# Kernel optimization log

Hardware: AMD Instinct MI355X
Metric: run time of the kernel (lower is better)

The kernel has to match this reference:

```python
import jax, jax.numpy as jnp
import numpy as np

N_NODES = 50000
N_EDGES = 800000
N_GRAPHS = 64
F0 = 64          # num_features
HID = 512        # hidden_size
N_OUT = 1


def setup_inputs() -> dict:
    key = jax.random.key(0)
    ks = jax.random.split(key, 16)

    def p(k, shape, scale):
        return jax.random.normal(k, shape, jnp.float32) * scale

    inp = {}
    inp["feature"] = jax.random.normal(ks[0], (N_NODES, F0), jnp.float32)
    inp["edge_index"] = jax.random.randint(ks[1], (2, N_EDGES), 0, N_NODES)
    inp["protein_batch"] = jnp.sort(jax.random.randint(ks[2], (N_NODES,), 0, N_GRAPHS))

    dims = [(F0, F0), (F0, 2 * F0), (2 * F0, 4 * F0)]
    for i, (din, dout) in enumerate(dims):
        s = 1.0 / np.sqrt(din)
        inp[f"W{i+1}"] = p(ks[3 + 3 * i], (din, dout), s)      # GATConv lin weight
        inp[f"att{i+1}"] = p(ks[4 + 3 * i], (2, dout), 0.1)    # [att_src; att_dst]
        inp[f"b{i+1}"] = jnp.zeros((dout,), jnp.float32)       # GATConv bias
    inp["fc1_w"] = p(ks[12], (4 * F0, HID), 1.0 / np.sqrt(4 * F0))
    inp["fc1_b"] = jnp.zeros((HID,), jnp.float32)
    inp["fc2_w"] = p(ks[13], (HID, N_OUT), 1.0 / np.sqrt(HID))
    inp["fc2_b"] = jnp.zeros((N_OUT,), jnp.float32)
    return inp


def _gat_conv(x, src, dst, W, att, b):
    """PyG GATConv, heads=1, concat=True, negative_slope=0.2 (self-loops already in src/dst)."""
    h = x @ W                                             # [N, Dout]
    # per-edge attention logit: a_src . h_j + a_dst . h_i
    alpha = jax.nn.leaky_relu(h @ att[0], 0.2 * 0 + 0.0)  # placeholder, replaced below
    logit = jax.nn.leaky_relu((h @ att[0])[src] + (h @ att[1])[dst], negative_slope=0.2)  # [E]
    # segment softmax over edges grouped by destination node
    m = jax.ops.segment_max(logit, dst, num_segments=N_NODES)      # [N]
    e = jnp.exp(logit - m[dst])                                    # [E]
    s = jax.ops.segment_sum(e, dst, num_segments=N_NODES)          # [N]
    coef = e / s[dst]                                              # [E]
    out = jax.ops.segment_sum(coef[:, None] * h[src], dst, num_segments=N_NODES)  # [N, Dout]
    return out + b


def reference(feature, edge_index, protein_batch,
              W1, att1, b1, W2, att2, b2, W3, att3, b3,
              fc1_w, fc1_b, fc2_w, fc2_b):
    loop = jnp.arange(N_NODES)
    src = jnp.concatenate([edge_index[0], loop])   # add_self_loops=True
    dst = jnp.concatenate([edge_index[1], loop])

    x = jax.nn.relu(_gat_conv(feature, src, dst, W1, att1, b1))
    x = jax.nn.relu(_gat_conv(x, src, dst, W2, att2, b2))
    x = jax.nn.relu(_gat_conv(x, src, dst, W3, att3, b3))

    # global mean pool per graph
    sums = jax.ops.segment_sum(x, protein_batch, num_segments=N_GRAPHS)          # [G, 4F]
    cnts = jax.ops.segment_sum(jnp.ones((N_NODES,), x.dtype), protein_batch,
                               num_segments=N_GRAPHS)                            # [G]
    gc = sums / jnp.maximum(cnts, 1.0)[:, None]

    gc = jax.nn.relu(gc @ fc1_w + fc1_b)   # dropout is identity at inference
    return gc @ fc2_w + fc2_b
```

## Files before the change

kernel.cpp:

```cpp
#include <hip/hip_runtime.h>
#include <hip/hip_bf16.h>

#define N_NODES 50000
#define N_EDGES 800000
#define E_TOT   850000
#define N_GRAPHS 64
#define HID 512

typedef unsigned short u16;
typedef __attribute__((ext_vector_type(8))) short short8;
typedef __attribute__((ext_vector_type(4))) float floatx4;
typedef union { uint4 u; short8 s; } frag_u;

__device__ inline unsigned f2b(float x) {
    unsigned u = __float_as_uint(x);
    return (u + 0x7fffu + ((u >> 16) & 1u)) >> 16;
}
__device__ inline float b2f_lo(unsigned u) { return __uint_as_float(u << 16); }
__device__ inline float b2f_hi(unsigned u) { return __uint_as_float(u & 0xffff0000u); }

__global__ __launch_bounds__(256) void count_kernel(const int* __restrict__ dst_e,
                                                    int* __restrict__ cnt,
                                                    int* __restrict__ order) {
    int e = blockIdx.x * 256 + threadIdx.x;
    if (e >= E_TOT) return;
    int d = (e < N_EDGES) ? dst_e[e] : (e - N_EDGES);
    order[e] = atomicAdd(&cnt[d], 1);
}

__global__ __launch_bounds__(256) void scan_local(const int* __restrict__ cnt,
                                                  int* __restrict__ out,
                                                  int* __restrict__ blocksum, int n) {
    __shared__ int buf[256];
    int tid = threadIdx.x;
    int i = blockIdx.x * 256 + tid;
    int v = (i < n) ? cnt[i] : 0;
    buf[tid] = v;
    __syncthreads();
    for (int off = 1; off < 256; off <<= 1) {
        int t = (tid >= off) ? buf[tid - off] : 0;
        __syncthreads();
        buf[tid] += t;
        __syncthreads();
    }
    if (i < n) out[i] = buf[tid] - v;
    if (tid == 255) blocksum[blockIdx.x] = buf[255];
}

__global__ __launch_bounds__(256) void scan_block(const int* __restrict__ blocksum,
                                                  int* __restrict__ blockoff, int nb,
                                                  int* __restrict__ total_ptr) {
    __shared__ int buf[256];
    int tid = threadIdx.x;
    int v = (tid < nb) ? blocksum[tid] : 0;
    buf[tid] = v;
    __syncthreads();
    for (int off = 1; off < 256; off <<= 1) {
        int t = (tid >= off) ? buf[tid - off] : 0;
        __syncthreads();
        buf[tid] += t;
        __syncthreads();
    }
    blockoff[tid] = buf[tid] - v;
    if (tid == 255) *total_ptr = buf[255];
}

__global__ __launch_bounds__(256) void scan_add(int* __restrict__ row_ptr,
                                                const int* __restrict__ blockoff, int n) {
    int i = blockIdx.x * 256 + threadIdx.x;
    if (i < n) row_ptr[i] += blockoff[blockIdx.x];
}

__global__ __launch_bounds__(256) void fill_kernel(const int* __restrict__ edge_index,
                                                   const int* __restrict__ row_ptr,
                                                   const int* __restrict__ order,
                                                   int* __restrict__ col_idx) {
    int e = blockIdx.x * 256 + threadIdx.x;
    if (e >= E_TOT) return;
    int s, d;
    if (e < N_EDGES) { s = edge_index[e]; d = edge_index[N_EDGES + e]; }
    else             { s = e - N_EDGES;   d = s; }
    col_idx[row_ptr[d] + order[e]] = s;
}

struct PrepDesc {
    const float* W[3];
    const float* att[3];
    float* wsd[3];
    u16* Wt[3];
};

__global__ __launch_bounds__(256) void prep_kernel(PrepDesc d) {
    const int DIN[3]  = {64, 64, 128};
    const int DOUT[3] = {64, 128, 256};
    int b = blockIdx.x;
    if (b < 128) {
        int wg = (b * 256 + (int)threadIdx.x) >> 6;
        int lane = threadIdx.x & 63;
        int l = (wg < 128) ? 0 : (wg < 256) ? 1 : 2;
        int base = (l == 0) ? 0 : (l == 1) ? 128 : 256;
        int k = wg - base;
        int Din = DIN[l], Dout = DOUT[l];
        int half = (k >= Din) ? 1 : 0;
        int row = half ? (k - Din) : k;
        float s = 0.f;
        for (int j = lane; j < Dout; j += 64)
            s += d.W[l][(size_t)row * Dout + j] * d.att[l][half * Dout + j];
#pragma unroll
        for (int off = 32; off > 0; off >>= 1) s += __shfl_xor(s, off);
        if (lane == 0) d.wsd[l][k] = s;
    } else {
        int t = (b - 128) * 256 + (int)threadIdx.x;
        int l; int off;
        if (t < 4096)       { l = 0; off = t; }
        else if (t < 12288) { l = 1; off = t - 4096; }
        else if (t < 45056) { l = 2; off = t - 12288; }
        else return;
        int Din = DIN[l], Dout = DOUT[l];
        int row = off / Dout, j = off & (Dout - 1);
        d.Wt[l][(size_t)j * Din + row] = (u16)f2b(d.W[l][off]);
    }
}

__global__ __launch_bounds__(256) void cvt_lsld_kernel(const float* __restrict__ feature,
                                                       const float* __restrict__ wsd,
                                                       u16* __restrict__ Fb,
                                                       float* __restrict__ lsld) {
    int wid = (blockIdx.x * 256 + threadIdx.x) >> 6;
    int lane = threadIdx.x & 63;
    if (wid >= N_NODES) return;
    float h = feature[(size_t)wid * 64 + lane];
    float a0 = h * wsd[lane];
    float a1 = h * wsd[64 + lane];
#pragma unroll
    for (int off = 32; off > 0; off >>= 1) {
        a0 += __shfl_xor(a0, off);
        a1 += __shfl_xor(a1, off);
    }
    if (lane == 0) { lsld[wid] = a0; lsld[N_NODES + wid] = a1; }
    Fb[(size_t)wid * 64 + lane] = (u16)f2b(h);
}

template <int NN, int KK>
__global__ __launch_bounds__(256) void sgemm_mfma_kernel(const u16* __restrict__ A,
                                                         const u16* __restrict__ Bt,
                                                         u16* __restrict__ C,
                                                         const float* __restrict__ bias,
                                                         const float* __restrict__ wsd_next,
                                                         float* __restrict__ lsld_next,
                                                         const int* __restrict__ batch,
                                                         float* __restrict__ gsum_pool,
                                                         int M) {
    constexpr int NT = 4;
    constexpr int KSTEPS = KK / 32;
    constexpr int CS = 72;
    __shared__ u16 cst[4][32 * CS];
    const int lane = threadIdx.x & 63;
    const int w = threadIdx.x >> 6;
    const int c = lane & 15;
    const int q = lane >> 4;
    const int bn = blockIdx.y * 64;
    const int r0 = blockIdx.x * 128 + w * 32;
    int ar0 = r0 + c;      if (ar0 > M - 1) ar0 = M - 1;
    int ar1 = r0 + 16 + c; if (ar1 > M - 1) ar1 = M - 1;
    const u16* __restrict__ Ap0 = A + (size_t)ar0 * KK + q * 8;
    const u16* __restrict__ Ap1 = A + (size_t)ar1 * KK + q * 8;
    floatx4 acc[2][NT];
#pragma unroll
    for (int i = 0; i < 2; ++i)
#pragma unroll
        for (int b = 0; b < NT; ++b) acc[i][b] = (floatx4){0.f, 0.f, 0.f, 0.f};
#pragma unroll
    for (int ks = 0; ks < KSTEPS; ++ks) {
        const int k0 = ks * 32;
        frag_u a0, a1, bf[NT];
        a0.u = *(const uint4*)(Ap0 + k0);
        a1.u = *(const uint4*)(Ap1 + k0);
#pragma unroll
        for (int b = 0; b < NT; ++b)
            bf[b].u = *(const uint4*)(Bt + (size_t)(bn + b * 16 + c) * KK + q * 8 + k0);
#pragma unroll
        for (int b = 0; b < NT; ++b) {
            acc[0][b] = __builtin_amdgcn_mfma_f32_16x16x32_bf16(a0.s, bf[b].s, acc[0][b], 0, 0, 0);
            acc[1][b] = __builtin_amdgcn_mfma_f32_16x16x32_bf16(a1.s, bf[b].s, acc[1][b], 0, 0, 0);
        }
    }

    if (gsum_pool) {
        float bsv[NT];
#pragma unroll
        for (int b = 0; b < NT; ++b) bsv[b] = bias[bn + b * 16 + c];
        const bool full = (r0 + 31 < M);
        const int rl = full ? (r0 + 31) : (M - 1);
        if (full && batch[r0] == batch[rl]) {
            const int gr = batch[r0];
#pragma unroll
            for (int b = 0; b < NT; ++b) {
                float s = 0.f;
#pragma unroll
                for (int i = 0; i < 2; ++i)
#pragma unroll
                    for (int g = 0; g < 4; ++g) s += fmaxf(acc[i][b][g] + bsv[b], 0.f);
                s += __shfl_xor(s, 16);
                s += __shfl_xor(s, 32);
                if (q == 0) atomicAdd(&gsum_pool[gr * 256 + bn + b * 16 + c], s);
            }
        } else {
#pragma unroll
            for (int i = 0; i < 2; ++i) {
                int curg = -1;
                float sb[NT] = {0.f, 0.f, 0.f, 0.f};
#pragma unroll
                for (int g = 0; g < 4; ++g) {
                    int r = r0 + i * 16 + q * 4 + g;
                    if (r < M) {
                        int gr = batch[r];
                        if (gr != curg) {
                            if (curg >= 0) {
#pragma unroll
                                for (int b = 0; b < NT; ++b) {
                                    atomicAdd(&gsum_pool[curg * 256 + bn + b * 16 + c], sb[b]);
                                    sb[b] = 0.f;
                                }
                            }
                            curg = gr;
                        }
#pragma unroll
                        for (int b = 0; b < NT; ++b) sb[b] += fmaxf(acc[i][b][g] + bsv[b], 0.f);
                    }
                }
                if (curg >= 0) {
#pragma unroll
                    for (int b = 0; b < NT; ++b)
                        atomicAdd(&gsum_pool[curg * 256 + bn + b * 16 + c], sb[b]);
                }
            }
        }
        return;
    }

    const bool has_next = (wsd_next != nullptr);
    u16* __restrict__ cb = cst[w];
    float ps[2][4] = {}, pd[2][4] = {};
#pragma unroll
    for (int b = 0; b < NT; ++b) {
        const int col = bn + b * 16 + c;
        const float bsv = bias[col];
        const float wsv = has_next ? wsd_next[col] : 0.f;
        const float wdv = has_next ? wsd_next[NN + col] : 0.f;
#pragma unroll
        for (int i = 0; i < 2; ++i) {
#pragma unroll
            for (int g = 0; g < 4; ++g) {
                float v = fmaxf(acc[i][b][g] + bsv, 0.f);
                cb[(i * 16 + q * 4 + g) * CS + b * 16 + c] = (u16)f2b(v);
                ps[i][g] += v * wsv;
                pd[i][g] += v * wdv;
            }
        }
    }
    if (has_next) {
#pragma unroll
        for (int i = 0; i < 2; ++i)
#pragma unroll
            for (int g = 0; g < 4; ++g) {
#pragma unroll
                for (int mm = 1; mm < 16; mm <<= 1) {
                    ps[i][g] += __shfl_xor(ps[i][g], mm);
                    pd[i][g] += __shfl_xor(pd[i][g], mm);
                }
            }
        if (c == 0) {
#pragma unroll
            for (int i = 0; i < 2; ++i)
#pragma unroll
                for (int g = 0; g < 4; ++g) {
                    int r = r0 + i * 16 + q * 4 + g;
                    if (r < M) {
                        atomicAdd(&lsld_next[r], ps[i][g]);
                        atomicAdd(&lsld_next[M + r], pd[i][g]);
                    }
                }
        }
    }
#pragma unroll
    for (int p = 0; p < 4; ++p) {
        int lr = p * 8 + (lane >> 3);
        int r = r0 + lr;
        if (r < M) {
            uint4 val = *(const uint4*)&cb[lr * CS + (lane & 7) * 8];
            *(uint4*)(C + (size_t)r * NN + bn + (lane & 7) * 8) = val;
        }
    }
}

template <int D>
__global__ __launch_bounds__(256) void gather_fused_kernel(const u16* __restrict__ X,
                                                           const float* __restrict__ lsld,
                                                           const int* __restrict__ row_ptr,
                                                           const int* __restrict__ col_idx,
                                                           u16* __restrict__ out) {
    constexpr int L = D / 8;
    constexpr int P = 64 / L;
    __shared__ float2 ec_all[4][64];
    int wid = (blockIdx.x * 256 + threadIdx.x) >> 6;
    int lane = threadIdx.x & 63;
    if (wid >= N_NODES) return;
    float2* __restrict__ ec = ec_all[threadIdx.x >> 6];
    const int start = row_ptr[wid];
    const int end = row_ptr[wid + 1];
    const int deg = end - start;
    const float ldi = lsld[N_NODES + wid];
    const float* __restrict__ ls = lsld;
    const int eslot = lane / L;
    const int fidx = lane % L;
    float a[8] = {0.f, 0.f, 0.f, 0.f, 0.f, 0.f, 0.f, 0.f};

    auto fma8 = [&](float cc, uint4 v) {
        a[0] += cc * b2f_lo(v.x); a[1] += cc * b2f_hi(v.x);
        a[2] += cc * b2f_lo(v.y); a[3] += cc * b2f_hi(v.y);
        a[4] += cc * b2f_lo(v.z); a[5] += cc * b2f_hi(v.z);
        a[6] += cc * b2f_lo(v.w); a[7] += cc * b2f_hi(v.w);
    };

    if (deg <= 64) {
        int srcl = 0;
        float l = -3.0e38f;
        if (lane < deg) {
            srcl = col_idx[start + lane];
            float t = ls[srcl] + ldi;
            l = (t > 0.f) ? t : 0.2f * t;
        }
        float m = l;
#pragma unroll
        for (int off = 32; off > 0; off >>= 1) m = fmaxf(m, __shfl_xor(m, off));
        float e = (lane < deg) ? __expf(l - m) : 0.f;
        float s = e;
#pragma unroll
        for (int off = 32; off > 0; off >>= 1) s += __shfl_xor(s, off);
        ec[lane] = make_float2(e / s, __int_as_float(srcl));

        const int nsteps = (deg + P - 1) / P;
        for (int g0 = 0; g0 < nsteps; g0 += 4) {
            float2 p[4]; uint4 v[4];
#pragma unroll
            for (int j = 0; j < 4; ++j) {
                int idx = (g0 + j) * P + eslot;
                bool valid = idx < deg;
                p[j] = ec[valid ? idx : 0];
                if (!valid) p[j].x = 0.f;
            }
#pragma unroll
            for (int j = 0; j < 4; ++j)
                v[j] = *(const uint4*)(X + (size_t)__float_as_int(p[j].y) * D + fidx * 8);
#pragma unroll
            for (int j = 0; j < 4; ++j) fma8(p[j].x, v[j]);
        }
    } else {
        float m = -3.0e38f;
        for (int e = start + lane; e < end; e += 64) {
            float t = ls[col_idx[e]] + ldi;
            t = (t > 0.f) ? t : 0.2f * t;
            m = fmaxf(m, t);
        }
#pragma unroll
        for (int off = 32; off > 0; off >>= 1) m = fmaxf(m, __shfl_xor(m, off));
        float ssum = 0.f;
        for (int e = start + lane; e < end; e += 64) {
            float t = ls[col_idx[e]] + ldi;
            t = (t > 0.f) ? t : 0.2f * t;
            ssum += __expf(t - m);
        }
#pragma unroll
        for (int off = 32; off > 0; off >>= 1) ssum += __shfl_xor(ssum, off);
        const float inv = 1.0f / ssum;
        for (int e0 = start; e0 < end; e0 += P) {
            int e = e0 + eslot;
            if (e < end) {
                int src = col_idx[e];
                float t = ls[src] + ldi;
                t = (t > 0.f) ? t : 0.2f * t;
                float cc = __expf(t - m) * inv;
                uint4 v = *(const uint4*)(X + (size_t)src * D + fidx * 8);
                fma8(cc, v);
            }
        }
    }
#pragma unroll
    for (int mm = L; mm < 64; mm <<= 1) {
#pragma unroll
        for (int i = 0; i < 8; ++i) a[i] += __shfl_xor(a[i], mm);
    }
    if (lane < L) {
        uint4 o;
        o.x = f2b(a[0]) | (f2b(a[1]) << 16);
        o.y = f2b(a[2]) | (f2b(a[3]) << 16);
        o.z = f2b(a[4]) | (f2b(a[5]) << 16);
        o.w = f2b(a[6]) | (f2b(a[7]) << 16);
        *(uint4*)(out + (size_t)wid * D + lane * 8) = o;
    }
}

__device__ inline int lower_bound_dev(const int* __restrict__ a, int n, int v) {
    int lo = 0, hi = n;
    while (lo < hi) { int mid = (lo + hi) >> 1; if (a[mid] < v) lo = mid + 1; else hi = mid; }
    return lo;
}

__global__ __launch_bounds__(256) void fc_kernel(const float* __restrict__ gsum,
                                                 const int* __restrict__ batch,
                                                 const float* __restrict__ w1,
                                                 const float* __restrict__ b1,
                                                 const float* __restrict__ w2,
                                                 const float* __restrict__ b2,
                                                 float* __restrict__ out) {
    __shared__ float gc[256];
    __shared__ float h1s[HID];
    __shared__ float red[256];
    __shared__ int s_cnt;
    int g = blockIdx.x;
    int tid = threadIdx.x;
    if (tid == 0)
        s_cnt = lower_bound_dev(batch, N_NODES, g + 1) - lower_bound_dev(batch, N_NODES, g);
    __syncthreads();
    float denom = fmaxf((float)s_cnt, 1.0f);
    gc[tid] = gsum[g * 256 + tid] / denom;
    __syncthreads();
#pragma unroll
    for (int jj = 0; jj < 2; ++jj) {
        int j = tid + jj * 256;
        float sum = b1[j];
        for (int k = 0; k < 256; ++k) sum += gc[k] * w1[k * HID + j];
        h1s[j] = (sum > 0.f) ? sum : 0.f;
    }
    __syncthreads();
    float acc = h1s[tid] * w2[tid] + h1s[tid + 256] * w2[tid + 256];
    red[tid] = acc;
    __syncthreads();
    for (int off = 128; off > 0; off >>= 1) {
        if (tid < off) red[tid] += red[tid + off];
        __syncthreads();
    }
    if (tid == 0) out[g] = red[0] + b2[0];
}

extern "C" void kernel_launch(void* const* d_in, const int* in_sizes, int n_in,
                              void* d_out, int out_size, void* d_ws, size_t ws_size,
                              hipStream_t stream) {
    const float* feature  = (const float*)d_in[0];
    const int*   edge_idx = (const int*)d_in[1];
    const int*   batch    = (const int*)d_in[2];
    const float* W1    = (const float*)d_in[3];
    const float* att1  = (const float*)d_in[4];
    const float* b1    = (const float*)d_in[5];
    const float* W2    = (const float*)d_in[6];
    const float* att2  = (const float*)d_in[7];
    const float* b2    = (const float*)d_in[8];
    const float* W3    = (const float*)d_in[9];
    const float* att3  = (const float*)d_in[10];
    const float* b3    = (const float*)d_in[11];
    const float* fc1_w = (const float*)d_in[12];
    const float* fc1_b = (const float*)d_in[13];
    const float* fc2_w = (const float*)d_in[14];
    const float* fc2_b = (const float*)d_in[15];
    float* out = (float*)d_out;

    char* w = (char*)d_ws;
    auto alloc = [&](size_t bytes) {
        char* p = w;
        w += (bytes + 255) & ~(size_t)255;
        return p;
    };
    u16* Fb    = (u16*)alloc((size_t)N_NODES * 64 * 2);
    u16* X1b   = (u16*)alloc((size_t)N_NODES * 64 * 2);
    u16* X2b   = (u16*)alloc((size_t)N_NODES * 128 * 2);
    u16* AGGb  = (u16*)alloc((size_t)N_NODES * 128 * 2);
    float* lsld1 = (float*)alloc((size_t)N_NODES * 2 * 4);
    char* zbase = w;
    int* cnt      = (int*)alloc((size_t)N_NODES * 4);
    float* gsum   = (float*)alloc(64 * 256 * 4);
    float* lsld23 = (float*)alloc((size_t)N_NODES * 4 * 4);
    size_t zbytes = (size_t)(w - zbase);
    float* lsld2 = lsld23;
    float* lsld3 = lsld23 + (size_t)N_NODES * 2;
    float* wsd1  = (float*)alloc(2 * 64 * 4);
    float* wsd2  = (float*)alloc(2 * 64 * 4);
    float* wsd3  = (float*)alloc(2 * 128 * 4);
    u16* Wt1   = (u16*)alloc(64 * 64 * 2);
    u16* Wt2   = (u16*)alloc(128 * 64 * 2);
    u16* Wt3   = (u16*)alloc(256 * 128 * 2);
    int* row_ptr  = (int*)alloc((size_t)(N_NODES + 1) * 4);
    int* col_idx  = (int*)alloc((size_t)E_TOT * 4);
    int* order    = (int*)alloc((size_t)E_TOT * 4);
    int* blocksum = (int*)alloc(256 * 4);
    int* blockoff = (int*)alloc(256 * 4);

    hipMemsetAsync(zbase, 0, zbytes, stream);

    const int EB = (E_TOT + 255) / 256;
    const int NB = (N_NODES + 255) / 256;
    const int WB = (N_NODES * 64 + 255) / 256;
    const int GB = (N_NODES + 127) / 128;

    PrepDesc pd;
    pd.W[0] = W1; pd.W[1] = W2; pd.W[2] = W3;
    pd.att[0] = att1; pd.att[1] = att2; pd.att[2] = att3;
    pd.wsd[0] = wsd1; pd.wsd[1] = wsd2; pd.wsd[2] = wsd3;
    pd.Wt[0] = Wt1; pd.Wt[1] = Wt2; pd.Wt[2] = Wt3;
    prep_kernel<<<304, 256, 0, stream>>>(pd);

    count_kernel<<<EB, 256, 0, stream>>>(edge_idx + N_EDGES, cnt, order);
    scan_local<<<NB, 256, 0, stream>>>(cnt, row_ptr, blocksum, N_NODES);
    scan_block<<<1, 256, 0, stream>>>(blocksum, blockoff, NB, row_ptr + N_NODES);
    scan_add<<<NB, 256, 0, stream>>>(row_ptr, blockoff, N_NODES);
    fill_kernel<<<EB, 256, 0, stream>>>(edge_idx, row_ptr, order, col_idx);

    cvt_lsld_kernel<<<WB, 256, 0, stream>>>(feature, wsd1, Fb, lsld1);
    gather_fused_kernel<64><<<WB, 256, 0, stream>>>(Fb, lsld1, row_ptr, col_idx, AGGb);
    sgemm_mfma_kernel<64, 64><<<dim3(GB, 1), 256, 0, stream>>>(AGGb, Wt1, X1b, b1, wsd2, lsld2, nullptr, nullptr, N_NODES);

    gather_fused_kernel<64><<<WB, 256, 0, stream>>>(X1b, lsld2, row_ptr, col_idx, AGGb);
    sgemm_mfma_kernel<128, 64><<<dim3(GB, 2), 256, 0, stream>>>(AGGb, Wt2, X2b, b2, wsd3, lsld3, nullptr, nullptr, N_NODES);

    gather_fused_kernel<128><<<WB, 256, 0, stream>>>(X2b, lsld3, row_ptr, col_idx, AGGb);
    sgemm_mfma_kernel<256, 128><<<dim3(GB, 4), 256, 0, stream>>>(AGGb, Wt3, nullptr, b3, nullptr, nullptr, batch, gsum, N_NODES);

    fc_kernel<<<N_GRAPHS, 256, 0, stream>>>(gsum, batch, fc1_w, fc1_b, fc2_w, fc2_b, out);
}
```

Before: 304.4 us.

## Merge CSR build and preprocessing kernels to cut launch count

Independent preprocessing kernels are merged into shared launches by splitting on block index: weight prep with edge counting, local scan with feature conversion, and the scan-add with the CSR fill. The fill now adds the block offset inline, and a second row_ptr buffer is written so the gathers read finalized offsets. This drops the number of kernel launches and serialization points from 8 to 4. The cost is an extra row_ptr buffer and an extra blockoff load in the fill.

```diff
diff --git a/kernel.cpp b/kernel.cpp
--- a/kernel.cpp
+++ b/kernel.cpp
@@ -6,6 +6,10 @@
 #define E_TOT   850000
 #define N_GRAPHS 64
 #define HID 512
+#define NBC 196
+#define PB  304
+#define EB  3321
+#define WB  12500
 
 typedef unsigned short u16;
 typedef __attribute__((ext_vector_type(8))) short short8;
@@ -18,70 +22,6 @@
 }
 __device__ inline float b2f_lo(unsigned u) { return __uint_as_float(u << 16); }
 __device__ inline float b2f_hi(unsigned u) { return __uint_as_float(u & 0xffff0000u); }
-
-__global__ __launch_bounds__(256) void count_kernel(const int* __restrict__ dst_e,
-                                                    int* __restrict__ cnt,
-                                                    int* __restrict__ order) {
-    int e = blockIdx.x * 256 + threadIdx.x;
-    if (e >= E_TOT) return;
-    int d = (e < N_EDGES) ? dst_e[e] : (e - N_EDGES);
-    order[e] = atomicAdd(&cnt[d], 1);
-}
-
-__global__ __launch_bounds__(256) void scan_local(const int* __restrict__ cnt,
-                                                  int* __restrict__ out,
-                                                  int* __restrict__ blocksum, int n) {
-    __shared__ int buf[256];
-    int tid = threadIdx.x;
-    int i = blockIdx.x * 256 + tid;
-    int v = (i < n) ? cnt[i] : 0;
-    buf[tid] = v;
-    __syncthreads();
-    for (int off = 1; off < 256; off <<= 1) {
-        int t = (tid >= off) ? buf[tid - off] : 0;
-        __syncthreads();
-        buf[tid] += t;
-        __syncthreads();
-    }
-    if (i < n) out[i] = buf[tid] - v;
-    if (tid == 255) blocksum[blockIdx.x] = buf[255];
-}
-
-__global__ __launch_bounds__(256) void scan_block(const int* __restrict__ blocksum,
-                                                  int* __restrict__ blockoff, int nb,
-                                                  int* __restrict__ total_ptr) {
-    __shared__ int buf[256];
-    int tid = threadIdx.x;
-    int v = (tid < nb) ? blocksum[tid] : 0;
-    buf[tid] = v;
-    __syncthreads();
-    for (int off = 1; off < 256; off <<= 1) {
-        int t = (tid >= off) ? buf[tid - off] : 0;
-        __syncthreads();
-        buf[tid] += t;
-        __syncthreads();
-    }
-    blockoff[tid] = buf[tid] - v;
-    if (tid == 255) *total_ptr = buf[255];
-}
-
-__global__ __launch_bounds__(256) void scan_add(int* __restrict__ row_ptr,
-                                                const int* __restrict__ blockoff, int n) {
-    int i = blockIdx.x * 256 + threadIdx.x;
-    if (i < n) row_ptr[i] += blockoff[blockIdx.x];
-}
-
-__global__ __launch_bounds__(256) void fill_kernel(const int* __restrict__ edge_index,
-                                                   const int* __restrict__ row_ptr,
-                                                   const int* __restrict__ order,
-                                                   int* __restrict__ col_idx) {
-    int e = blockIdx.x * 256 + threadIdx.x;
-    if (e >= E_TOT) return;
-    int s, d;
-    if (e < N_EDGES) { s = edge_index[e]; d = edge_index[N_EDGES + e]; }
-    else             { s = e - N_EDGES;   d = s; }
-    col_idx[row_ptr[d] + order[e]] = s;
-}
 
 struct PrepDesc {
     const float* W[3];
@@ -90,10 +30,20 @@
     u16* Wt[3];
 };
 
-__global__ __launch_bounds__(256) void prep_kernel(PrepDesc d) {
+__global__ __launch_bounds__(256) void prep_count_kernel(PrepDesc d,
+                                                         const int* __restrict__ dst_e,
+                                                         int* __restrict__ cnt,
+                                                         int* __restrict__ order) {
     const int DIN[3]  = {64, 64, 128};
     const int DOUT[3] = {64, 128, 256};
     int b = blockIdx.x;
+    if (b >= PB) {
+        int e = (b - PB) * 256 + threadIdx.x;
+        if (e >= E_TOT) return;
+        int dd = (e < N_EDGES) ? dst_e[e] : (e - N_EDGES);
+        order[e] = atomicAdd(&cnt[dd], 1);
+        return;
+    }
     if (b < 128) {
         int wg = (b * 256 + (int)threadIdx.x) >> 6;
         int lane = threadIdx.x & 63;
@@ -122,23 +72,80 @@
     }
 }
 
-__global__ __launch_bounds__(256) void cvt_lsld_kernel(const float* __restrict__ feature,
-                                                       const float* __restrict__ wsd,
+__global__ __launch_bounds__(256) void scan_cvt_kernel(const int* __restrict__ cnt,
+                                                       int* __restrict__ row_ptr,
+                                                       int* __restrict__ blocksum,
+                                                       const float* __restrict__ feature,
+                                                       const float* __restrict__ wsd1,
                                                        u16* __restrict__ Fb,
-                                                       float* __restrict__ lsld) {
-    int wid = (blockIdx.x * 256 + threadIdx.x) >> 6;
-    int lane = threadIdx.x & 63;
-    if (wid >= N_NODES) return;
-    float h = feature[(size_t)wid * 64 + lane];
-    float a0 = h * wsd[lane];
-    float a1 = h * wsd[64 + lane];
-#pragma unroll
-    for (int off = 32; off > 0; off >>= 1) {
-        a0 += __shfl_xor(a0, off);
-        a1 += __shfl_xor(a1, off);
-    }
-    if (lane == 0) { lsld[wid] = a0; lsld[N_NODES + wid] = a1; }
-    Fb[(size_t)wid * 64 + lane] = (u16)f2b(h);
+                                                       float* __restrict__ lsld1) {
+    if (blockIdx.x < NBC) {
+        __shared__ int buf[256];
+        int tid = threadIdx.x;
+        int i = blockIdx.x * 256 + tid;
+        int v = (i < N_NODES) ? cnt[i] : 0;
+        buf[tid] = v;
+        __syncthreads();
+        for (int off = 1; off < 256; off <<= 1) {
+            int t = (tid >= off) ? buf[tid - off] : 0;
+            __syncthreads();
+            buf[tid] += t;
+            __syncthreads();
+        }
+        if (i < N_NODES) row_ptr[i] = buf[tid] - v;
+        if (tid == 255) blocksum[blockIdx.x] = buf[255];
+    } else {
+        int wid = ((blockIdx.x - NBC) * 256 + (int)threadIdx.x) >> 6;
+        int lane = threadIdx.x & 63;
+        if (wid >= N_NODES) return;
+        float h = feature[(size_t)wid * 64 + lane];
+        float a0 = h * wsd1[lane];
+        float a1 = h * wsd1[64 + lane];
+#pragma unroll
+        for (int off = 32; off > 0; off >>= 1) {
+            a0 += __shfl_xor(a0, off);
+            a1 += __shfl_xor(a1, off);
+        }
+        if (lane == 0) { lsld1[wid] = a0; lsld1[N_NODES + wid] = a1; }
+        Fb[(size_t)wid * 64 + lane] = (u16)f2b(h);
+    }
+}
+
+__global__ __launch_bounds__(256) void scan_block_kernel(const int* __restrict__ blocksum,
+                                                         int* __restrict__ blockoff,
+                                                         int* __restrict__ row_ptr2_last) {
+    __shared__ int buf[256];
+    int tid = threadIdx.x;
+    int v = (tid < NBC) ? blocksum[tid] : 0;
+    buf[tid] = v;
+    __syncthreads();
+    for (int off = 1; off < 256; off <<= 1) {
+        int t = (tid >= off) ? buf[tid - off] : 0;
+        __syncthreads();
+        buf[tid] += t;
+        __syncthreads();
+    }
+    blockoff[tid] = buf[tid] - v;
+    if (tid == 255) *row_ptr2_last = buf[255];
+}
+
+__global__ __launch_bounds__(256) void fin_fill_kernel(const int* __restrict__ edge_index,
+                                                       const int* __restrict__ row_ptr,
+                                                       const int* __restrict__ blockoff,
+                                                       const int* __restrict__ order,
+                                                       int* __restrict__ col_idx,
+                                                       int* __restrict__ row_ptr2) {
+    if (blockIdx.x < NBC) {
+        int i = blockIdx.x * 256 + threadIdx.x;
+        if (i < N_NODES) row_ptr2[i] = row_ptr[i] + blockoff[blockIdx.x];
+        return;
+    }
+    int e = (blockIdx.x - NBC) * 256 + threadIdx.x;
+    if (e >= E_TOT) return;
+    int s, d;
+    if (e < N_EDGES) { s = edge_index[e]; d = edge_index[N_EDGES + e]; }
+    else             { s = e - N_EDGES;   d = s; }
+    col_idx[row_ptr[d] + blockoff[d >> 8] + order[e]] = s;
 }
 
 template <int NN, int KK>
@@ -489,7 +496,8 @@
     u16* Wt1   = (u16*)alloc(64 * 64 * 2);
     u16* Wt2   = (u16*)alloc(128 * 64 * 2);
     u16* Wt3   = (u16*)alloc(256 * 128 * 2);
-    int* row_ptr  = (int*)alloc((size_t)(N_NODES + 1) * 4);
+    int* row_ptr  = (int*)alloc((size_t)N_NODES * 4);
+    int* row_ptr2 = (int*)alloc((size_t)(N_NODES + 1) * 4);
     int* col_idx  = (int*)alloc((size_t)E_TOT * 4);
     int* order    = (int*)alloc((size_t)E_TOT * 4);
     int* blocksum = (int*)alloc(256 * 4);
@@ -497,9 +505,6 @@
 
     hipMemsetAsync(zbase, 0, zbytes, stream);
 
-    const int EB = (E_TOT + 255) / 256;
-    const int NB = (N_NODES + 255) / 256;
-    const int WB = (N_NODES * 64 + 255) / 256;
     const int GB = (N_NODES + 127) / 128;
 
     PrepDesc pd;
@@ -507,22 +512,19 @@
     pd.att[0] = att1; pd.att[1] = att2; pd.att[2] = att3;
     pd.wsd[0] = wsd1; pd.wsd[1] = wsd2; pd.wsd[2] = wsd3;
     pd.Wt[0] = Wt1; pd.Wt[1] = Wt2; pd.Wt[2] = Wt3;
-    prep_kernel<<<304, 256, 0, stream>>>(pd);
-
-    count_kernel<<<EB, 256, 0, stream>>>(edge_idx + N_EDGES, cnt, order);
-    scan_local<<<NB, 256, 0, stream>>>(cnt, row_ptr, blocksum, N_NODES);
-    scan_block<<<1, 256, 0, stream>>>(blocksum, blockoff, NB, row_ptr + N_NODES);
-    scan_add<<<NB, 256, 0, stream>>>(row_ptr, blockoff, N_NODES);
-    fill_kernel<<<EB, 256, 0, stream>>>(edge_idx, row_ptr, order, col_idx);
-
-    cvt_lsld_kernel<<<WB, 256, 0, stream>>>(feature, wsd1, Fb, lsld1);
-    gather_fused_kernel<64><<<WB, 256, 0, stream>>>(Fb, lsld1, row_ptr, col_idx, AGGb);
+
+    prep_count_kernel<<<PB + EB, 256, 0, stream>>>(pd, edge_idx + N_EDGES, cnt, order);
+    scan_cvt_kernel<<<NBC + WB, 256, 0, stream>>>(cnt, row_ptr, blocksum, feature, wsd1, Fb, lsld1);
+    scan_block_kernel<<<1, 256, 0, stream>>>(blocksum, blockoff, row_ptr2 + N_NODES);
+    fin_fill_kernel<<<NBC + EB, 256, 0, stream>>>(edge_idx, row_ptr, blockoff, order, col_idx, row_ptr2);
+
+    gather_fused_kernel<64><<<WB, 256, 0, stream>>>(Fb, lsld1, row_ptr2, col_idx, AGGb);
     sgemm_mfma_kernel<64, 64><<<dim3(GB, 1), 256, 0, stream>>>(AGGb, Wt1, X1b, b1, wsd2, lsld2, nullptr, nullptr, N_NODES);
 
-    gather_fused_kernel<64><<<WB, 256, 0, stream>>>(X1b, lsld2, row_ptr, col_idx, AGGb);
+    gather_fused_kernel<64><<<WB, 256, 0, stream>>>(X1b, lsld2, row_ptr2, col_idx, AGGb);
     sgemm_mfma_kernel<128, 64><<<dim3(GB, 2), 256, 0, stream>>>(AGGb, Wt2, X2b, b2, wsd3, lsld3, nullptr, nullptr, N_NODES);
 
-    gather_fused_kernel<128><<<WB, 256, 0, stream>>>(X2b, lsld3, row_ptr, col_idx, AGGb);
+    gather_fused_kernel<128><<<WB, 256, 0, stream>>>(X2b, lsld3, row_ptr2, col_idx, AGGb);
     sgemm_mfma_kernel<256, 128><<<dim3(GB, 4), 256, 0, stream>>>(AGGb, Wt3, nullptr, b3, nullptr, nullptr, batch, gsum, N_NODES);
 
     fc_kernel<<<N_GRAPHS, 256, 0, stream>>>(gsum, batch, fc1_w, fc1_b, fc2_w, fc2_b, out);
```

After: 299.8 us. Within noise of the previous version (-1.5%).
